# Kernel optimization log

Hardware: AMD Instinct MI355X
Metric: run time of the kernel (lower is better)

## Reference

```python
import jax, jax.numpy as jnp
import numpy as np

B, S, D, H, HD = 1, 2048, 1024, 16, 64
WINDOW = 512
RADIUS = max(1, WINDOW // 2)
GLOBAL_IDX = (0, 1, 2, 3)
NEG = -1e9


def rotate_half(x):
    x1, x2 = jnp.split(x, 2, axis=-1)
    return jnp.concatenate([-x2, x1], axis=-1)


def apply_rope(x, cos, sin, pos):
    # x: [b, s, h, hd]; cos/sin: [max_pos, hd]; pos: [b, s]
    c = cos[pos][:, :, None, :]
    s_ = sin[pos][:, :, None, :]
    return x * c + rotate_half(x) * s_


def setup_inputs() -> dict:
    key = jax.random.key(0)
    ks = jax.random.split(key, 12)
    x = jax.random.normal(ks[0], (B, S, D), dtype=jnp.float32)
    # RoPE tables (standard construction)
    inv_freq = 1.0 / (10000.0 ** (jnp.arange(0, HD, 2, dtype=jnp.float32) / HD))
    t = jnp.arange(S, dtype=jnp.float32)
    freqs = jnp.outer(t, inv_freq)                      # [S, HD/2]
    emb = jnp.concatenate([freqs, freqs], axis=-1)      # [S, HD]
    cos_freqs = jnp.cos(emb)
    sin_freqs = jnp.sin(emb)
    position_ids = jnp.broadcast_to(jnp.arange(S, dtype=jnp.int32), (B, S))
    w = lambda k: jax.random.normal(k, (D, D), dtype=jnp.float32) * 0.02
    return {
        "x": x, "cos_freqs": cos_freqs, "sin_freqs": sin_freqs,
        "position_ids": position_ids,
        "Wqs": w(ks[1]), "Wks": w(ks[2]), "Wvs": w(ks[3]),
        "Wqg": w(ks[4]), "Wkg": w(ks[5]), "Wvg": w(ks[6]),
        "Wo": w(ks[7]),
    }


def reference(x, cos_freqs, sin_freqs, position_ids, Wqs, Wks, Wvs, Wqg, Wkg, Wvg, Wo):
    b, s, d = x.shape
    split = lambda y: y.reshape(b, s, H, HD)
    qs = split(x @ Wqs)
    ks_ = split(x @ Wks)
    vs = split(x @ Wvs)
    kg = split(x @ Wkg)
    vg = split(x @ Wvg)
    # (qg projection exists in the module but is unused by its forward math)
    qs = apply_rope(qs, cos_freqs, sin_freqs, position_ids)
    ks_ = apply_rope(ks_, cos_freqs, sin_freqs, position_ids)

    qs_t = jnp.swapaxes(qs, 1, 2)   # [b,h,s,hd]
    ks_t = jnp.swapaxes(ks_, 1, 2)
    vs_t = jnp.swapaxes(vs, 1, 2)
    scale = 1.0 / jnp.sqrt(jnp.float32(HD))

    # local sliding-window (causal) attention over dense scores
    scores = jnp.einsum('bhsd,bhtd->bhst', qs_t, ks_t) * scale
    i = jnp.arange(s)[:, None]
    j = jnp.arange(s)[None, :]
    mask = (jnp.abs(i - j) <= RADIUS) & (j <= i)
    scores = jnp.where(mask[None, None], scores, NEG)
    g = jnp.array(GLOBAL_IDX)
    scores = scores.at[:, :, :, g].add(1e9)  # same as per-index set(score+1e9)
    attn = jax.nn.softmax(scores, axis=-1)
    out_local = jnp.einsum('bhst,bhtd->bhsd', attn, vs_t)
    out_local = jnp.swapaxes(out_local, 1, 2).reshape(b, s, d)

    # global attention: all queries attend to the global-index columns of kg/vg
    kg_t = jnp.swapaxes(kg, 1, 2)
    vg_t = jnp.swapaxes(vg, 1, 2)
    scores_g = jnp.einsum('bhsd,bhtd->bhst', qs_t, kg_t) * scale
    col_mask = jnp.zeros((s,), dtype=bool).at[g].set(True)
    scores_g = jnp.where(col_mask[None, None, None, :], scores_g, NEG)
    attn_g = jax.nn.softmax(scores_g, axis=-1)
    out_global = jnp.einsum('bhst,bhtd->bhsd', attn_g, vg_t)
    out_global = jnp.swapaxes(out_global, 1, 2).reshape(b, s, d)

    return (out_local + out_global) @ Wo
```

## Files before the change

### kernel.cpp

```cpp
#include <hip/hip_runtime.h>

typedef _Float16 half8 __attribute__((ext_vector_type(8)));
typedef float floatx4 __attribute__((ext_vector_type(4)));

#define SEQ 2048
#define DMODEL 1024
#define NHEADS 16
#define HEADDIM 64
#define PW 5120

__global__ __launch_bounds__(256) void k_prep(
    const float* __restrict__ x,
    const float* __restrict__ w0, const float* __restrict__ w1, const float* __restrict__ w2,
    const float* __restrict__ w3, const float* __restrict__ w4, const float* __restrict__ w5,
    _Float16* __restrict__ xh, _Float16* __restrict__ wcat, _Float16* __restrict__ wot) {
  const int tid = threadIdx.x;
  const int b = blockIdx.x;
  if (b < 1024) {
    int base = b * 2048 + tid * 8;
    floatx4 f0 = *(const floatx4*)(x + base);
    floatx4 f1 = *(const floatx4*)(x + base + 4);
    half8 h;
    #pragma unroll
    for (int e = 0; e < 4; ++e) { h[e] = (_Float16)f0[e]; h[e + 4] = (_Float16)f1[e]; }
    *(half8*)(xh + base) = h;
    return;
  }
  __shared__ _Float16 T[64][72];
  int t = b - 1024;
  int z = t >> 8;
  int tile = t & 255;
  int k0 = (tile >> 4) * 64, n0 = (tile & 15) * 64;
  const float* W = (z == 0) ? w0 : (z == 1) ? w1 : (z == 2) ? w2
                 : (z == 3) ? w3 : (z == 4) ? w4 : w5;
  _Float16* dst = (z < 5) ? (wcat + (size_t)z * 1024 * 1024) : wot;

  int lr = tid >> 2, c0 = (tid & 3) * 16;
  #pragma unroll
  for (int i = 0; i < 4; ++i) {
    floatx4 f = *(const floatx4*)(W + (size_t)(k0 + lr) * DMODEL + n0 + c0 + i * 4);
    #pragma unroll
    for (int e = 0; e < 4; ++e) T[c0 + i * 4 + e][lr] = (_Float16)f[e];
  }
  __syncthreads();
  int nr = tid >> 2, s0 = (tid & 3) * 16;
  #pragma unroll
  for (int i = 0; i < 2; ++i) {
    half8 h = *(const half8*)&T[nr][s0 + i * 8];
    *(half8*)(dst + (size_t)(n0 + nr) * DMODEL + k0 + s0 + i * 8) = h;
  }
}

template <bool HALF_OUT, bool FUSE_ROPE, bool SPARSE>
__global__ __launch_bounds__(256, 3) void k_gemm(
    const _Float16* __restrict__ A, const _Float16* __restrict__ Bt,
    void* __restrict__ Cv, float* __restrict__ Cp,
    const float* __restrict__ cos_t, const float* __restrict__ sin_t,
    const int* __restrict__ pos, int M, int N, int K) {
  __shared__ _Float16 As[128][128];
  __shared__ _Float16 Bs[64][128];
  const int tid = threadIdx.x;
  const int lane = tid & 63;
  const int w = tid >> 6;
  const int wm = w * 32;
  const int l15 = lane & 15;
  const int q4 = lane >> 4;
  int m0, n0;
  if (SPARSE) {
    int b = blockIdx.x;
    if (b < 768) { m0 = (b & 15) * 128; n0 = (b >> 4) * 64; }
    else         { m0 = 0;              n0 = 3072 + (b - 768) * 64; }
  } else {
    m0 = blockIdx.x * 128;
    n0 = blockIdx.y * 64;
  }

  floatx4 acc[2][4];
  #pragma unroll
  for (int i = 0; i < 2; ++i)
    #pragma unroll
    for (int j = 0; j < 4; ++j) acc[i][j] = (floatx4){0.f, 0.f, 0.f, 0.f};

  _Float16* asBase = &As[0][0];
  _Float16* bsBase = &Bs[0][0];
  const int swz = l15 & 7;

  for (int k0 = 0; k0 < K; k0 += 128) {
    __syncthreads();
    #pragma unroll
    for (int it = 0; it < 8; ++it) {
      int c = it * 256 + tid;
      int r = c >> 4, cc = c & 15;
      int g = cc ^ (r & 7);
      __builtin_amdgcn_global_load_lds(
          (const __attribute__((address_space(1))) void*)(A + (size_t)(m0 + r) * K + k0 + g * 8),
          (__attribute__((address_space(3))) void*)(asBase + (it * 256 + w * 64) * 8),
          16, 0, 0);
    }
    #pragma unroll
    for (int it = 0; it < 4; ++it) {
      int c = it * 256 + tid;
      int r = c >> 4, cc = c & 15;
      int g = cc ^ (r & 7);
      __builtin_amdgcn_global_load_lds(
          (const __attribute__((address_space(1))) void*)(Bt + (size_t)(n0 + r) * K + k0 + g * 8),
          (__attribute__((address_space(3))) void*)(bsBase + (it * 256 + w * 64) * 8),
          16, 0, 0);
    }
    __syncthreads();

    #pragma unroll
    for (int kk = 0; kk < 4; ++kk) {
      int q = kk * 4 + q4;
      half8 af[2], bf[4];
      #pragma unroll
      for (int t = 0; t < 2; ++t) {
        int ar = wm + t * 16 + l15;
        af[t] = *(const half8*)(asBase + (size_t)ar * 128 + ((q ^ swz) * 8));
      }
      #pragma unroll
      for (int t = 0; t < 4; ++t) {
        int br = t * 16 + l15;
        bf[t] = *(const half8*)(bsBase + (size_t)br * 128 + ((q ^ swz) * 8));
      }
      #pragma unroll
      for (int i = 0; i < 2; ++i)
        #pragma unroll
        for (int j = 0; j < 4; ++j)
          acc[i][j] = __builtin_amdgcn_mfma_f32_16x16x32_f16(af[i], bf[j], acc[i][j], 0, 0, 0);
    }
  }

  #pragma unroll
  for (int tm = 0; tm < 2; ++tm) {
    #pragma unroll
    for (int r = 0; r < 4; ++r) {
      int row = m0 + wm + tm * 16 + q4 * 4 + r;
      float v[4];
      #pragma unroll
      for (int tn = 0; tn < 4; ++tn) v[tn] = acc[tm][tn][r];
      if (FUSE_ROPE && n0 < 2048) {
        int p = pos[row];
        #pragma unroll
        for (int tn = 0; tn < 2; ++tn) {
          int d = tn * 16 + l15;
          float a = acc[tm][tn][r];
          float bvv = acc[tm][tn + 2][r];
          float c1 = cos_t[p * 64 + d],      s1 = sin_t[p * 64 + d];
          float c2 = cos_t[p * 64 + d + 32], s2 = sin_t[p * 64 + d + 32];
          v[tn]     = a * c1 - bvv * s1;
          v[tn + 2] = bvv * c2 + a * s2;
        }
      }
      #pragma unroll
      for (int tn = 0; tn < 4; ++tn) {
        int col = n0 + tn * 16 + l15;
        if (HALF_OUT)
          ((_Float16*)Cv)[(size_t)row * N + col] = (_Float16)v[tn];
        else
          Cp[(size_t)row * N + col] = v[tn];
      }
    }
  }
}

__global__ __launch_bounds__(256, 2) void k_attn(const _Float16* __restrict__ proj,
                                                 _Float16* __restrict__ out) {
  const int tid = threadIdx.x;
  const int hb = blockIdx.y * 64;

  if (blockIdx.x >= 28) {
    const int i = (blockIdx.x - 28) * 4 + (tid >> 6);
    const int lane = tid & 63;
    const float scale = 0.125f;
    float qv = (float)proj[(size_t)i * PW + hb + lane];
    float sg[4];
    #pragma unroll
    for (int g = 0; g < 4; ++g) {
      float kgv = (float)proj[(size_t)g * PW + 3072 + hb + lane];
      float v = qv * kgv;
      #pragma unroll
      for (int off = 32; off; off >>= 1) v += __shfl_xor(v, off, 64);
      sg[g] = v * scale;
    }
    float mg = fmaxf(fmaxf(sg[0], sg[1]), fmaxf(sg[2], sg[3]));
    float dg = 0.f, og = 0.f;
    #pragma unroll
    for (int g = 0; g < 4; ++g) {
      float p = __expf(sg[g] - mg);
      dg += p;
      og += p * (float)proj[(size_t)g * PW + 4096 + hb + lane];
    }
    og /= dg;
    int jmin = (i >= 256) ? (i - 256) : 0;
    int jmax = (i < 3) ? i : 3;
    float acc = 0.f;
    for (int j = jmin; j <= jmax; ++j)
      acc += (float)proj[(size_t)j * PW + 2048 + hb + lane];
    float ol = acc / (float)(jmax - jmin + 1);
    out[(size_t)i * DMODEL + hb + lane] = (_Float16)(ol + og);
    return;
  }

  const int i0 = 256 + blockIdx.x * 64;
  const int jlo = i0 - 256;
  const int lane = tid & 63;
  const int w = tid >> 6;
  const int l15 = lane & 15;
  const int q4 = lane >> 4;

  __shared__ _Float16 Qs[64][72];
  __shared__ _Float16 Kc[64][72];
  __shared__ _Float16 Vtc[64][72];
  __shared__ _Float16 Ps[64][72];
  __shared__ _Float16 kg_s[4][64];
  __shared__ _Float16 vg_s[4][64];
  __shared__ float svg_s[64];
  __shared__ float pg_s[4][64];

  #pragma unroll
  for (int rep = 0; rep < 2; ++rep) {
    int c = tid + rep * 256;
    int r = c >> 3, q = c & 7;
    *(half8*)&Qs[r][q * 8] = *(const half8*)(proj + (size_t)(i0 + r) * PW + hb + q * 8);
  }
  {
    int g = tid >> 6, c2 = tid & 63;
    kg_s[g][c2] = proj[(size_t)g * PW + 3072 + hb + c2];
    vg_s[g][c2] = proj[(size_t)g * PW + 4096 + hb + c2];
    if (tid < 64) {
      float s = 0.f;
      #pragma unroll
      for (int g2 = 0; g2 < 4; ++g2) s += (float)proj[(size_t)g2 * PW + 2048 + hb + tid];
      svg_s[tid] = s;
    }
  }
  __syncthreads();

  {
    int ro = w * 16 + (lane >> 2);
    int part = lane & 3;
    float sg[4];
    #pragma unroll
    for (int g = 0; g < 4; ++g) {
      float acc = 0.f;
      #pragma unroll
      for (int u = 0; u < 16; ++u)
        acc += (float)Qs[ro][part * 16 + u] * (float)kg_s[g][part * 16 + u];
      acc += __shfl_xor(acc, 1, 64);
      acc += __shfl_xor(acc, 2, 64);
      sg[g] = acc * 0.125f;
    }
    float mg = fmaxf(fmaxf(sg[0], sg[1]), fmaxf(sg[2], sg[3]));
    float dg = 0.f;
    #pragma unroll
    for (int g = 0; g < 4; ++g) dg += __expf(sg[g] - mg);
    pg_s[part][ro] = __expf(sg[part] - mg) / dg;
  }

  half8 qf0 = *(const half8*)&Qs[w * 16 + l15][q4 * 8];
  half8 qf1 = *(const half8*)&Qs[w * 16 + l15][32 + q4 * 8];

  float lpart[4];
  floatx4 oacc[4];
  #pragma unroll
  for (int cb = 0; cb < 4; ++cb) {
    oacc[cb] = (floatx4){0.f, 0.f, 0.f, 0.f};
    lpart[cb] = 0.f;
  }

  const int kr_r0 = tid >> 3, kr_q = tid & 7;
  const int kr_r1 = kr_r0 + 32;
  const int vj0 = (tid & 7) + ((tid >> 6) << 3);
  const int vj1 = vj0 + 32;
  const int vd0 = ((tid >> 3) & 7) * 8;

  half8 kr0, kr1, vr0, vr1;
  {
    const _Float16* kb = proj + (size_t)jlo * PW + 1024 + hb;
    const _Float16* vb = proj + (size_t)jlo * PW + 2048 + hb;
    kr0 = *(const half8*)(kb + (size_t)kr_r0 * PW + kr_q * 8);
    kr1 = *(const half8*)(kb + (size_t)kr_r1 * PW + kr_q * 8);
    vr0 = *(const half8*)(vb + (size_t)vj0 * PW + vd0);
    vr1 = *(const half8*)(vb + (size_t)vj1 * PW + vd0);
  }

  for (int cc = 0; cc < 5; ++cc) {
    __syncthreads();
    *(half8*)&Kc[kr_r0][kr_q * 8] = kr0;
    *(half8*)&Kc[kr_r1][kr_q * 8] = kr1;
    #pragma unroll
    for (int u = 0; u < 8; ++u) {
      int d = vd0 + u;
      Vtc[d][vj0 ^ (d & 56)] = vr0[u];
      Vtc[d][vj1 ^ (d & 56)] = vr1[u];
    }
    if (cc < 4) {
      const _Float16* kb = proj + (size_t)(jlo + (cc + 1) * 64) * PW + 1024 + hb;
      const _Float16* vb = proj + (size_t)(jlo + (cc + 1) * 64) * PW + 2048 + hb;
      kr0 = *(const half8*)(kb + (size_t)kr_r0 * PW + kr_q * 8);
      kr1 = *(const half8*)(kb + (size_t)kr_r1 * PW + kr_q * 8);
      vr0 = *(const half8*)(vb + (size_t)vj0 * PW + vd0);
      vr1 = *(const half8*)(vb + (size_t)vj1 * PW + vd0);
    }
    __syncthreads();

    float sc[4][4];
    #pragma unroll
    for (int cb = 0; cb < 4; ++cb) {
      half8 b0 = *(const half8*)&Kc[cb * 16 + l15][q4 * 8];
      half8 b1 = *(const half8*)&Kc[cb * 16 + l15][32 + q4 * 8];
      floatx4 a = (floatx4){0.f, 0.f, 0.f, 0.f};
      a = __builtin_amdgcn_mfma_f32_16x16x32_f16(qf0, b0, a, 0, 0, 0);
      a = __builtin_amdgcn_mfma_f32_16x16x32_f16(qf1, b1, a, 0, 0, 0);
      #pragma unroll
      for (int r = 0; r < 4; ++r) sc[cb][r] = a[r];
    }

    #pragma unroll
    for (int r = 0; r < 4; ++r) {
      int ri = w * 16 + q4 * 4 + r;
      float rowp = 0.f;
      #pragma unroll
      for (int cb = 0; cb < 4; ++cb) {
        int jjg = cc * 64 + cb * 16 + l15;
        bool valid = (jjg >= ri) && (jjg <= ri + 256);
        float p = valid ? __expf(sc[cb][r] * 0.125f) : 0.f;
        Ps[ri][cb * 16 + l15] = (_Float16)p;
        rowp += p;
      }
      lpart[r] += rowp;
    }

    half8 pf0 = *(const half8*)&Ps[w * 16 + l15][q4 * 8];
    half8 pf1 = *(const half8*)&Ps[w * 16 + l15][32 + q4 * 8];
    #pragma unroll
    for (int cb = 0; cb < 4; ++cb) {
      int dv = cb * 16 + l15;
      half8 v0 = *(const half8*)&Vtc[dv][(q4 * 8) ^ (dv & 56)];
      half8 v1 = *(const half8*)&Vtc[dv][(32 + q4 * 8) ^ (dv & 56)];
      oacc[cb] = __builtin_amdgcn_mfma_f32_16x16x32_f16(pf0, v0, oacc[cb], 0, 0, 0);
      oacc[cb] = __builtin_amdgcn_mfma_f32_16x16x32_f16(pf1, v1, oacc[cb], 0, 0, 0);
    }
  }

  #pragma unroll
  for (int r = 0; r < 4; ++r) {
    int ri = w * 16 + q4 * 4 + r;
    if (i0 + ri < 260) continue;
    float lsum = lpart[r];
    #pragma unroll
    for (int off = 1; off < 16; off <<= 1) lsum += __shfl_xor(lsum, off, 64);
    float inv = 1.f / (lsum + 4.f);
    #pragma unroll
    for (int cb = 0; cb < 4; ++cb) {
      int col = cb * 16 + l15;
      float ol = (oacc[cb][r] + svg_s[col]) * inv;
      float og = 0.f;
      #pragma unroll
      for (int g = 0; g < 4; ++g) og += pg_s[g][ri] * (float)vg_s[g][col];
      out[(size_t)(i0 + ri) * DMODEL + hb + col] = (_Float16)(ol + og);
    }
  }
}

extern "C" void kernel_launch(void* const* d_in, const int* in_sizes, int n_in,
                              void* d_out, int out_size, void* d_ws, size_t ws_size,
                              hipStream_t stream) {
  const float* x     = (const float*)d_in[0];
  const float* cos_t = (const float*)d_in[1];
  const float* sin_t = (const float*)d_in[2];
  const int*   pos   = (const int*)d_in[3];
  const float* Wqs   = (const float*)d_in[4];
  const float* Wks   = (const float*)d_in[5];
  const float* Wvs   = (const float*)d_in[6];
  const float* Wkg   = (const float*)d_in[8];
  const float* Wvg   = (const float*)d_in[9];
  const float* Wo    = (const float*)d_in[10];
  float* out = (float*)d_out;

  char* ws = (char*)d_ws;
  _Float16* xh   = (_Float16*)(ws);
  _Float16* wcat = (_Float16*)(ws + (4u << 20));
  _Float16* wot  = (_Float16*)(ws + (14u << 20));
  _Float16* proj = (_Float16*)(ws + (16u << 20));
  _Float16* attn = (_Float16*)(ws + (36u << 20));

  k_prep<<<2560, 256, 0, stream>>>(x, Wqs, Wks, Wvs, Wkg, Wvg, Wo, xh, wcat, wot);
  k_gemm<true, true, true><<<800, 256, 0, stream>>>(
      xh, wcat, proj, nullptr, cos_t, sin_t, pos, SEQ, PW, DMODEL);
  k_attn<<<dim3(93, NHEADS), 256, 0, stream>>>(proj, attn);
  k_gemm<false, false, false><<<dim3(16, 16), 256, 0, stream>>>(
      attn, wot, nullptr, out, cos_t, sin_t, pos, SEQ, DMODEL, DMODEL);
}
```

Before: 157.0 us.

## Double-buffer GEMM K-tiles and widen projection tile to 128 columns

Restructures the fp16 MFMA GEMM into a two-stage LDS pipeline with 64-wide K tiles. The next tile's async global-to-LDS loads are issued before computing the current one, gated by vmcnt waits and raw barriers. Warps now form a 2x2 layout of 64-row tiles. The projection GEMM uses 128-column blocks, halving its grid to 400 blocks, while the output GEMM keeps 64-column blocks. The aim is to hide global load latency and raise reuse per block, at the cost of more registers, occupancy lowered to 2 blocks per CU, and fewer blocks to spread across CUs.

```diff
diff --git a/kernel.cpp b/kernel.cpp
--- a/kernel.cpp
+++ b/kernel.cpp
@@ -51,95 +51,117 @@
   }
 }
 
-template <bool HALF_OUT, bool FUSE_ROPE, bool SPARSE>
-__global__ __launch_bounds__(256, 3) void k_gemm(
+template <bool HALF_OUT, bool FUSE_ROPE, bool SPARSE, int BNT>
+__global__ __launch_bounds__(256, 2) void k_gemm(
     const _Float16* __restrict__ A, const _Float16* __restrict__ Bt,
     void* __restrict__ Cv, float* __restrict__ Cp,
     const float* __restrict__ cos_t, const float* __restrict__ sin_t,
     const int* __restrict__ pos, int M, int N, int K) {
-  __shared__ _Float16 As[128][128];
-  __shared__ _Float16 Bs[64][128];
+  __shared__ _Float16 As[2][128][64];
+  __shared__ _Float16 Bs[2][BNT][64];
   const int tid = threadIdx.x;
   const int lane = tid & 63;
   const int w = tid >> 6;
-  const int wm = w * 32;
   const int l15 = lane & 15;
   const int q4 = lane >> 4;
+  const int wm = (w >> 1) * 64;
+  const int wn = (w & 1) * (BNT / 2);
+  constexpr int NJ = BNT / 32;
   int m0, n0;
   if (SPARSE) {
     int b = blockIdx.x;
-    if (b < 768) { m0 = (b & 15) * 128; n0 = (b >> 4) * 64; }
-    else         { m0 = 0;              n0 = 3072 + (b - 768) * 64; }
+    if (b < 384) { m0 = (b & 15) * 128; n0 = (b >> 4) * 128; }
+    else         { m0 = 0;              n0 = 3072 + (b - 384) * 128; }
   } else {
     m0 = blockIdx.x * 128;
-    n0 = blockIdx.y * 64;
-  }
-
-  floatx4 acc[2][4];
-  #pragma unroll
-  for (int i = 0; i < 2; ++i)
-    #pragma unroll
-    for (int j = 0; j < 4; ++j) acc[i][j] = (floatx4){0.f, 0.f, 0.f, 0.f};
-
-  _Float16* asBase = &As[0][0];
-  _Float16* bsBase = &Bs[0][0];
+    n0 = blockIdx.y * BNT;
+  }
+
+  floatx4 acc[4][NJ];
+  #pragma unroll
+  for (int i = 0; i < 4; ++i)
+    #pragma unroll
+    for (int j = 0; j < NJ; ++j) acc[i][j] = (floatx4){0.f, 0.f, 0.f, 0.f};
+
   const int swz = l15 & 7;
 
-  for (int k0 = 0; k0 < K; k0 += 128) {
-    __syncthreads();
-    #pragma unroll
-    for (int it = 0; it < 8; ++it) {
-      int c = it * 256 + tid;
-      int r = c >> 4, cc = c & 15;
+  const int cA = tid;
+  auto stageA = [&](int bufi, int k0) {
+    _Float16* ab = &As[bufi][0][0];
+    #pragma unroll
+    for (int it = 0; it < 4; ++it) {
+      int c = it * 256 + cA;
+      int r = c >> 3, cc = c & 7;
       int g = cc ^ (r & 7);
       __builtin_amdgcn_global_load_lds(
           (const __attribute__((address_space(1))) void*)(A + (size_t)(m0 + r) * K + k0 + g * 8),
-          (__attribute__((address_space(3))) void*)(asBase + (it * 256 + w * 64) * 8),
+          (__attribute__((address_space(3))) void*)(ab + (it * 256 + w * 64) * 8),
           16, 0, 0);
     }
-    #pragma unroll
-    for (int it = 0; it < 4; ++it) {
-      int c = it * 256 + tid;
-      int r = c >> 4, cc = c & 15;
+  };
+  auto stageB = [&](int bufi, int k0) {
+    _Float16* bb = &Bs[bufi][0][0];
+    #pragma unroll
+    for (int it = 0; it < NJ; ++it) {
+      int c = it * 256 + cA;
+      int r = c >> 3, cc = c & 7;
       int g = cc ^ (r & 7);
       __builtin_amdgcn_global_load_lds(
           (const __attribute__((address_space(1))) void*)(Bt + (size_t)(n0 + r) * K + k0 + g * 8),
-          (__attribute__((address_space(3))) void*)(bsBase + (it * 256 + w * 64) * 8),
+          (__attribute__((address_space(3))) void*)(bb + (it * 256 + w * 64) * 8),
           16, 0, 0);
     }
-    __syncthreads();
-
-    #pragma unroll
-    for (int kk = 0; kk < 4; ++kk) {
+  };
+
+  const int nt = K >> 6;
+  stageA(0, 0);
+  stageB(0, 0);
+  for (int t = 0; t < nt; ++t) {
+    const int cur = t & 1;
+    if (t + 1 < nt) {
+      stageA(cur ^ 1, (t + 1) << 6);
+      stageB(cur ^ 1, (t + 1) << 6);
+      if (BNT == 128) asm volatile("s_waitcnt vmcnt(8)" ::: "memory");
+      else            asm volatile("s_waitcnt vmcnt(6)" ::: "memory");
+    } else {
+      asm volatile("s_waitcnt vmcnt(0)" ::: "memory");
+    }
+    __builtin_amdgcn_s_barrier();
+
+    const _Float16* ab = &As[cur][0][0];
+    const _Float16* bb = &Bs[cur][0][0];
+    #pragma unroll
+    for (int kk = 0; kk < 2; ++kk) {
       int q = kk * 4 + q4;
-      half8 af[2], bf[4];
-      #pragma unroll
-      for (int t = 0; t < 2; ++t) {
-        int ar = wm + t * 16 + l15;
-        af[t] = *(const half8*)(asBase + (size_t)ar * 128 + ((q ^ swz) * 8));
+      half8 af[4], bf[NJ];
+      #pragma unroll
+      for (int tt = 0; tt < 4; ++tt) {
+        int ar = wm + tt * 16 + l15;
+        af[tt] = *(const half8*)(ab + (size_t)ar * 64 + ((q ^ swz) * 8));
       }
       #pragma unroll
-      for (int t = 0; t < 4; ++t) {
-        int br = t * 16 + l15;
-        bf[t] = *(const half8*)(bsBase + (size_t)br * 128 + ((q ^ swz) * 8));
+      for (int j = 0; j < NJ; ++j) {
+        int br = wn + j * 16 + l15;
+        bf[j] = *(const half8*)(bb + (size_t)br * 64 + ((q ^ swz) * 8));
       }
       #pragma unroll
-      for (int i = 0; i < 2; ++i)
+      for (int i = 0; i < 4; ++i)
         #pragma unroll
-        for (int j = 0; j < 4; ++j)
+        for (int j = 0; j < NJ; ++j)
           acc[i][j] = __builtin_amdgcn_mfma_f32_16x16x32_f16(af[i], bf[j], acc[i][j], 0, 0, 0);
     }
-  }
-
-  #pragma unroll
-  for (int tm = 0; tm < 2; ++tm) {
+    __builtin_amdgcn_s_barrier();
+  }
+
+  #pragma unroll
+  for (int tm = 0; tm < 4; ++tm) {
     #pragma unroll
     for (int r = 0; r < 4; ++r) {
       int row = m0 + wm + tm * 16 + q4 * 4 + r;
-      float v[4];
-      #pragma unroll
-      for (int tn = 0; tn < 4; ++tn) v[tn] = acc[tm][tn][r];
-      if (FUSE_ROPE && n0 < 2048) {
+      float v[NJ];
+      #pragma unroll
+      for (int tn = 0; tn < NJ; ++tn) v[tn] = acc[tm][tn][r];
+      if (FUSE_ROPE && BNT == 128 && n0 < 2048) {
         int p = pos[row];
         #pragma unroll
         for (int tn = 0; tn < 2; ++tn) {
@@ -153,8 +175,8 @@
         }
       }
       #pragma unroll
-      for (int tn = 0; tn < 4; ++tn) {
-        int col = n0 + tn * 16 + l15;
+      for (int tn = 0; tn < NJ; ++tn) {
+        int col = n0 + wn + tn * 16 + l15;
         if (HALF_OUT)
           ((_Float16*)Cv)[(size_t)row * N + col] = (_Float16)v[tn];
         else
@@ -387,9 +409,9 @@
   _Float16* attn = (_Float16*)(ws + (36u << 20));
 
   k_prep<<<2560, 256, 0, stream>>>(x, Wqs, Wks, Wvs, Wkg, Wvg, Wo, xh, wcat, wot);
-  k_gemm<true, true, true><<<800, 256, 0, stream>>>(
+  k_gemm<true, true, true, 128><<<400, 256, 0, stream>>>(
       xh, wcat, proj, nullptr, cos_t, sin_t, pos, SEQ, PW, DMODEL);
   k_attn<<<dim3(93, NHEADS), 256, 0, stream>>>(proj, attn);
-  k_gemm<false, false, false><<<dim3(16, 16), 256, 0, stream>>>(
+  k_gemm<false, false, false, 64><<<dim3(16, 16), 256, 0, stream>>>(
       attn, wot, nullptr, out, cos_t, sin_t, pos, SEQ, DMODEL, DMODEL);
 }
```

Measured after the change: 161.2 us. 2.7% more time.
